# Optimization experiments

Hardware: AMD Instinct MI355X
Metric: run time of the kernel (lower is better)

The kernel has to match this reference:

```python
import jax, jax.numpy as jnp
import numpy as np

N, E, B = 20000, 60000, 512
F_IN, ED, H, C = 7, 3, 4, 256
HC = H * C  # 1024
D_MODEL = 1024
EPS_BN = 1e-5


def setup_inputs() -> dict:
    key = jax.random.key(0)
    ks = jax.random.split(key, 24)
    s = 0.05
    inp = {
        'x': jax.random.normal(ks[0], (N, F_IN), jnp.float32),
        'edge_index': jax.random.randint(ks[1], (2, E), 0, N, jnp.int32),
        'edge_attr': jax.random.normal(ks[2], (E, ED), jnp.float32),
        'batch': jnp.sort(jax.random.randint(ks[3], (N,), 0, B, jnp.int32)),
        'w0': jax.random.normal(ks[4], (F_IN, HC), jnp.float32) * s,
        'w_rest': jax.random.normal(ks[5], (3, HC, HC), jnp.float32) * s,
        'w_edge': jax.random.normal(ks[6], (4, ED, HC), jnp.float32) * s,
        'att_src': jax.random.normal(ks[7], (4, H, C), jnp.float32) * s,
        'att_dst': jax.random.normal(ks[8], (4, H, C), jnp.float32) * s,
        'att_edge': jax.random.normal(ks[9], (4, H, C), jnp.float32) * s,
        'bias012': jax.random.normal(ks[10], (3, HC), jnp.float32) * s,
        'bias3': jax.random.normal(ks[11], (C,), jnp.float32) * s,
        'bn_gamma': jnp.ones((3, HC), jnp.float32),
        'bn_beta': jnp.zeros((3, HC), jnp.float32),
        'bn_mean': jnp.zeros((3, HC), jnp.float32),
        'bn_var': jnp.ones((3, HC), jnp.float32),
        'gate_w': jax.random.normal(ks[12], (C, 1), jnp.float32) * s,
        'gate_b': jnp.zeros((1,), jnp.float32),
        'proj_w': jax.random.normal(ks[13], (C, D_MODEL), jnp.float32) * s,
        'proj_b': jnp.zeros((D_MODEL,), jnp.float32),
    }
    return inp


def _gat_layer(x, ei, ea, W, We, a_s, a_d, a_e, bias, concat):
    # PyG GATConv with edge_dim, add_self_loops=True (fill_value='mean'), eval mode (no dropout)
    n = x.shape[0]
    sl = jnp.arange(n, dtype=ei.dtype)
    ea_mean = ea.mean(axis=0)
    ei = jnp.concatenate([ei, jnp.stack([sl, sl])], axis=1)            # [2, E+N]
    ea = jnp.concatenate([ea, jnp.broadcast_to(ea_mean, (n, ea.shape[1]))], axis=0)
    h = (x @ W).reshape(n, H, C)                                       # [N,H,C]
    alpha_src = jnp.einsum('nhc,hc->nh', h, a_s)
    alpha_dst = jnp.einsum('nhc,hc->nh', h, a_d)
    eh = (ea @ We).reshape(-1, H, C)
    alpha_e = jnp.einsum('ehc,hc->eh', eh, a_e)
    src, dst = ei[0], ei[1]
    alpha = jax.nn.leaky_relu(alpha_src[src] + alpha_dst[dst] + alpha_e, 0.2)  # [E+N,H]
    amax = jax.ops.segment_max(alpha, dst, num_segments=n)
    alpha = jnp.exp(alpha - amax[dst])
    denom = jax.ops.segment_sum(alpha, dst, num_segments=n)
    alpha = alpha / (denom[dst] + 1e-16)
    msg = h[src] * alpha[:, :, None]                                   # [E+N,H,C]
    out = jax.ops.segment_sum(msg, dst, num_segments=n)                # [N,H,C]
    out = out.reshape(n, H * C) if concat else out.mean(axis=1)
    return out + bias


def reference(x, edge_index, edge_attr, batch, w0, w_rest, w_edge, att_src, att_dst,
              att_edge, bias012, bias3, bn_gamma, bn_beta, bn_mean, bn_var,
              gate_w, gate_b, proj_w, proj_b):
    h = x
    for i in range(4):
        W = w0 if i == 0 else w_rest[i - 1]
        concat = i < 3
        b = bias012[i] if concat else bias3
        h = _gat_layer(h, edge_index, edge_attr, W, w_edge[i],
                       att_src[i], att_dst[i], att_edge[i], b, concat)
        if i < 3:
            # BatchNorm1d in eval mode, then ReLU (dropout is identity in eval)
            h = (h - bn_mean[i]) * (bn_gamma[i] / jnp.sqrt(bn_var[i] + EPS_BN)) + bn_beta[i]
            h = jax.nn.relu(h)
    # AttentionalAggregation: segment softmax over gate scores, weighted sum per graph
    gate = h @ gate_w + gate_b                                         # [N,1]
    gmax = jax.ops.segment_max(gate, batch, num_segments=B)
    g = jnp.exp(gate - gmax[batch])
    gsum = jax.ops.segment_sum(g, batch, num_segments=B)
    w = g / (gsum[batch] + 1e-16)
    graph = jax.ops.segment_sum(w * h, batch, num_segments=B)          # [B,256]
    return graph @ proj_w + proj_b                                     # [B,1024]
```

## Files before the change

### kernel.cpp

```cpp
#include <hip/hip_runtime.h>
#include <math.h>

#define NN 20000
#define NP 20480
#define EE 60000
#define BB 512
#define HC 1024
#define HH 4
#define CC 256

typedef _Float16 f16;
typedef f16 half8 __attribute__((ext_vector_type(8)));
typedef f16 f16x4 __attribute__((ext_vector_type(4)));
typedef float floatx4 __attribute__((ext_vector_type(4)));
typedef float floatx16 __attribute__((ext_vector_type(16)));

__device__ __forceinline__ size_t af_off(int n, int c) {
    int mblk = n >> 7, rr = n & 127;
    int iter = c >> 5, kc = c & 31;
    int kh = kc >> 4, kg = (kc >> 3) & 1, e = kc & 7;
    return ((((size_t)(mblk * 32 + iter) * 2 + kh) * 4 + (rr >> 5)) * 64 +
            (kg * 32 + (rr & 31))) * 8 + e;
}

__device__ __forceinline__ int node_remap(int bid) {
    return (bid >> 3) + (bid & 7) * 2500;
}

__device__ __forceinline__ void gload16(const f16* g, f16* l) {
    __builtin_amdgcn_global_load_lds((const __attribute__((address_space(1))) void*)g,
                                     (__attribute__((address_space(3))) void*)l, 16, 0, 0);
}

__global__ void ehist_kernel(const float* __restrict__ ea, const int* __restrict__ ei,
                             float* sums, int* counts, int E_) {
    int e = blockIdx.x * 256 + threadIdx.x;
    float s0 = 0.f, s1 = 0.f, s2 = 0.f;
    if (e < E_) {
        atomicAdd(&counts[ei[E_ + e]], 1);
        s0 = ea[e * 3 + 0];
        s1 = ea[e * 3 + 1];
        s2 = ea[e * 3 + 2];
    }
    for (int o = 32; o; o >>= 1) {
        s0 += __shfl_down(s0, o);
        s1 += __shfl_down(s1, o);
        s2 += __shfl_down(s2, o);
    }
    if ((threadIdx.x & 63) == 0) {
        atomicAdd(&sums[0], s0);
        atomicAdd(&sums[1], s1);
        atomicAdd(&sums[2], s2);
    }
}

__global__ void scan1_kernel(const int* __restrict__ counts, int* __restrict__ partial,
                             int* __restrict__ psums, int n) {
    __shared__ int sdata[256];
    int t = threadIdx.x;
    int i = blockIdx.x * 256 + t;
    int v = (i < n) ? counts[i] : 0;
    sdata[t] = v;
    __syncthreads();
#pragma unroll
    for (int off = 1; off < 256; off <<= 1) {
        int tmp = (t >= off) ? sdata[t - off] : 0;
        __syncthreads();
        sdata[t] += tmp;
        __syncthreads();
    }
    if (i < n) partial[i] = sdata[t];
    if (t == 255) psums[blockIdx.x] = sdata[255];
}

__global__ void scan2_kernel(int* __restrict__ psums, int nb) {
    __shared__ int sdata[128];
    int t = threadIdx.x;
    sdata[t] = (t < nb) ? psums[t] : 0;
    __syncthreads();
#pragma unroll
    for (int off = 1; off < 128; off <<= 1) {
        int tmp = (t >= off) ? sdata[t - off] : 0;
        __syncthreads();
        sdata[t] += tmp;
        __syncthreads();
    }
    if (t < nb) psums[t] = (t == 0) ? 0 : sdata[t - 1];
}

__global__ void scan3_kernel(const int* __restrict__ partial, const int* __restrict__ psums,
                             int* __restrict__ indptr, int n) {
    int i = blockIdx.x * 256 + threadIdx.x;
    if (i == 0) indptr[0] = 0;
    if (i < n) indptr[i + 1] = partial[i] + psums[blockIdx.x];
}

__global__ void scatter_kernel(const int* __restrict__ ei, const int* __restrict__ indptr,
                               int* fill, int* sorted, int* sdst, int E_) {
    int e = blockIdx.x * 256 + threadIdx.x;
    if (e >= E_) return;
    int d = ei[E_ + e];
    int pos = indptr[d] + atomicAdd(&fill[d], 1);
    sorted[pos] = e;
    sdst[pos] = d;
}

__global__ void bptr_kernel(const int* __restrict__ batch, int* bptr, int n, int nb) {
    int i = blockIdx.x * 256 + threadIdx.x;
    if (i >= n) return;
    int b = batch[i];
    if (i == 0) {
        for (int bb = 0; bb <= b; bb++) bptr[bb] = 0;
    } else {
        int pb = batch[i - 1];
        if (pb != b) {
            for (int bb = pb + 1; bb <= b; bb++) bptr[bb] = i;
        }
    }
    if (i == n - 1) {
        for (int bb = b + 1; bb <= nb; bb++) bptr[bb] = n;
    }
}

__global__ void prep0_kernel(const float* __restrict__ w_rest, f16* __restrict__ Bf,
                             const float* __restrict__ att_src,
                             const float* __restrict__ att_dst,
                             const float* __restrict__ w0,
                             const float* __restrict__ bias012, const float* __restrict__ bn_g,
                             const float* __restrict__ bn_b, const float* __restrict__ bn_m,
                             const float* __restrict__ bn_v,
                             const float* __restrict__ w_edge,
                             const float* __restrict__ att_edge,
                             const float* __restrict__ ea_sums,
                             float* __restrict__ wsv, float* __restrict__ wdv,
                             float* __restrict__ w0s, float* __restrict__ w0d,
                             float2* __restrict__ bnss,
                             float* __restrict__ Mmat, float* __restrict__ ae_self,
                             float invE) {
    int bid = blockIdx.x;
    int t = threadIdx.x;
    if (bid < 768) {
        __shared__ float tile[64][65];
        int bx = (bid & 15) * 64;
        int by = ((bid >> 4) & 15) * 64;
        int l = bid >> 8;
        int tr = t >> 6, tc = t & 63;
#pragma unroll
        for (int i = 0; i < 16; i++) {
            int r = by + i * 4 + tr;
            tile[i * 4 + tr][tc] = w_rest[(size_t)l * 1048576 + (size_t)r * 1024 + bx + tc];
        }
        __syncthreads();
        f16* bl = Bf + (size_t)l * 1048576;
#pragma unroll
        for (int ii = 0; ii < 2; ii++) {
            int idx = ii * 256 + t;
            int nl = idx >> 3, kg8 = idx & 7;
            int n = bx + nl, k = by + kg8 * 8;
            half8 v;
#pragma unroll
            for (int e = 0; e < 8; e++) v[e] = (f16)tile[kg8 * 8 + e][nl];
            *(half8*)&bl[af_off(n, k)] = v;
        }
    } else if (bid < 3840) {
        int b = bid - 768;
        int l = b >> 10, k = b & 1023;
        int hp = t >> 6, lane = t & 63;
        int col = hp * 256 + lane * 4;
        const float* wrow = w_rest + (size_t)l * 1048576 + (size_t)k * 1024;
        float4 w4 = *(const float4*)&wrow[col];
        float4 a4 = *(const float4*)&att_src[(l + 1) * HC + col];
        float4 d4 = *(const float4*)&att_dst[(l + 1) * HC + col];
        float sp = w4.x * a4.x + w4.y * a4.y + w4.z * a4.z + w4.w * a4.w;
        float dp = w4.x * d4.x + w4.y * d4.y + w4.z * d4.z + w4.w * d4.w;
        for (int m = 1; m < 64; m <<= 1) {
            sp += __shfl_xor(sp, m);
            dp += __shfl_xor(dp, m);
        }
        if (lane == 0) {
            wsv[((size_t)l * 1024 + k) * 4 + hp] = sp;
            wdv[((size_t)l * 1024 + k) * 4 + hp] = dp;
        }
    } else if (bid < 3847) {
        int f = bid - 3840;
        int hp = t >> 6, lane = t & 63;
        int col = hp * 256 + lane * 4;
        float4 w4 = *(const float4*)&w0[f * HC + col];
        float4 a4 = *(const float4*)&att_src[col];
        float4 d4 = *(const float4*)&att_dst[col];
        float sp = w4.x * a4.x + w4.y * a4.y + w4.z * a4.z + w4.w * a4.w;
        float dp = w4.x * d4.x + w4.y * d4.y + w4.z * d4.z + w4.w * d4.w;
        for (int m = 1; m < 64; m <<= 1) {
            sp += __shfl_xor(sp, m);
            dp += __shfl_xor(dp, m);
        }
        if (lane == 0) {
            w0s[f * 4 + hp] = sp;
            w0d[f * 4 + hp] = dp;
        }
    } else if (bid < 3859) {
        int i = (bid - 3847) * 256 + t;
        if (i < 3 * HC) {
            float s = bn_g[i] * rsqrtf(bn_v[i] + 1e-5f);
            float2 o;
            o.x = s;
            o.y = (bias012[i] - bn_m[i]) * s + bn_b[i];
            bnss[i] = o;
        }
    } else {
        __shared__ float red[256];
        __shared__ float Ms[12];
        int l = bid - 3859;
        for (int dh = 0; dh < 12; dh++) {
            int d = dh >> 2, hh = dh & 3;
            float v = w_edge[l * 3072 + d * HC + hh * CC + t] *
                      att_edge[l * HC + hh * CC + t];
            red[t] = v;
            __syncthreads();
            for (int o = 128; o; o >>= 1) {
                if (t < o) red[t] += red[t + o];
                __syncthreads();
            }
            if (t == 0) {
                Ms[dh] = red[0];
                Mmat[l * 12 + dh] = red[0];
            }
            __syncthreads();
        }
        if (t < 4) {
            float v = 0.f;
            for (int d = 0; d < 3; d++) v += ea_sums[d] * invE * Ms[d * 4 + t];
            ae_self[l * 4 + t] = v;
        }
    }
}

__global__ void prep2_kernel(const int* __restrict__ ei, const int* __restrict__ sorted,
                             const float* __restrict__ ea, const float* __restrict__ Mmat,
                             int* __restrict__ ssrc, float* __restrict__ aeh_pk,
                             const float* __restrict__ x, const float* __restrict__ w0s,
                             const float* __restrict__ w0d, float* __restrict__ asrc,
                             float* __restrict__ adst, float* __restrict__ xpad) {
    int bid = blockIdx.x;
    int t = threadIdx.x;
    if (bid < 235) {
        int idx = bid * 256 + t;
        if (idx >= EE) return;
        int eid = sorted[idx];
        ssrc[idx] = ei[eid];
        float a0 = ea[eid * 3 + 0], a1 = ea[eid * 3 + 1], a2 = ea[eid * 3 + 2];
#pragma unroll
        for (int l = 0; l < 4; l++) {
#pragma unroll
            for (int h = 0; h < 4; h++) {
                aeh_pk[(size_t)idx * 16 + l * 4 + h] =
                    a0 * Mmat[l * 12 + h] + a1 * Mmat[l * 12 + 4 + h] +
                    a2 * Mmat[l * 12 + 8 + h];
            }
        }
    } else {
        int n = (bid - 235) * 256 + t;
        if (n >= NN) return;
        float xr[7];
#pragma unroll
        for (int f = 0; f < 7; f++) xr[f] = x[n * 7 + f];
        float4 p0, p1;
        p0.x = xr[0]; p0.y = xr[1]; p0.z = xr[2]; p0.w = xr[3];
        p1.x = xr[4]; p1.y = xr[5]; p1.z = xr[6]; p1.w = 0.f;
        *(float4*)&xpad[(size_t)n * 8] = p0;
        *(float4*)&xpad[(size_t)n * 8 + 4] = p1;
#pragma unroll
        for (int hp = 0; hp < 4; hp++) {
            float s = 0.f, d = 0.f;
#pragma unroll
            for (int f = 0; f < 7; f++) {
                s += xr[f] * w0s[f * 4 + hp];
                d += xr[f] * w0d[f * 4 + hp];
            }
            asrc[n * 4 + hp] = s;
            adst[n * 4 + hp] = d;
        }
    }
}

__global__ void edgep_kernel(const int* __restrict__ ssrc, const int* __restrict__ sdst,
                             const float* __restrict__ aeh_pk, const float* __restrict__ asrc,
                             const float* __restrict__ adst, float* __restrict__ pe,
                             int layer) {
    int i = blockIdx.x * 256 + threadIdx.x;
    if (i >= EE) return;
    int src = ssrc[i];
    int dst = sdst[i];
    float4 a = *(const float4*)&asrc[(size_t)src * 4];
    float4 d = *(const float4*)&adst[(size_t)dst * 4];
    float4 m = *(const float4*)&aeh_pk[(size_t)i * 16 + layer * 4];
    float r[4] = {a.x + d.x + m.x, a.y + d.y + m.y, a.z + d.z + m.z, a.w + d.w + m.w};
    float4 o;
#pragma unroll
    for (int k = 0; k < 4; k++) {
        float v = (r[k] > 0.f) ? r[k] : 0.2f * r[k];
        (&o.x)[k] = __expf(v);
    }
    *(float4*)&pe[(size_t)i * 4] = o;
}

__global__ void agg0x_kernel(const float* __restrict__ xpad, const float* __restrict__ asrc,
                             const float* __restrict__ adst, const float* __restrict__ ae_self,
                             const int* __restrict__ ssrc, const float* __restrict__ pe,
                             const int* __restrict__ indptr, float* __restrict__ xagg) {
    int n = blockIdx.x * 256 + threadIdx.x;
    if (n >= NN) return;
    float4 as4 = *(const float4*)&asrc[(size_t)n * 4];
    float4 ad4 = *(const float4*)&adst[(size_t)n * 4];
    float adl[4] = {ad4.x, ad4.y, ad4.z, ad4.w};
    float asl[4] = {as4.x, as4.y, as4.z, as4.w};
    float4 x0 = *(const float4*)&xpad[(size_t)n * 8];
    float4 x1 = *(const float4*)&xpad[(size_t)n * 8 + 4];
    float xr[7] = {x0.x, x0.y, x0.z, x0.w, x1.x, x1.y, x1.z};
    float denom[4];
    float xa[4][7];
#pragma unroll
    for (int h = 0; h < 4; h++) {
        float r = asl[h] + adl[h] + ae_self[h];
        r = (r > 0.f) ? r : 0.2f * r;
        float p = __expf(r);
        denom[h] = p;
#pragma unroll
        for (int f = 0; f < 7; f++) xa[h][f] = p * xr[f];
    }
    int s = indptr[n], e = indptr[n + 1];
    for (int idx = s; idx < e; idx++) {
        int src = ssrc[idx];
        float4 pv = *(const float4*)&pe[(size_t)idx * 4];
        float pl[4] = {pv.x, pv.y, pv.z, pv.w};
        float4 s0 = *(const float4*)&xpad[(size_t)src * 8];
        float4 s1 = *(const float4*)&xpad[(size_t)src * 8 + 4];
        float xs[7] = {s0.x, s0.y, s0.z, s0.w, s1.x, s1.y, s1.z};
#pragma unroll
        for (int h = 0; h < 4; h++) {
            denom[h] += pl[h];
#pragma unroll
            for (int f = 0; f < 7; f++) xa[h][f] += pl[h] * xs[f];
        }
    }
#pragma unroll
    for (int h = 0; h < 4; h++) {
        float inv = 1.0f / (denom[h] + 1e-16f);
#pragma unroll
        for (int f = 0; f < 7; f++) xagg[(size_t)n * 28 + h * 7 + f] = xa[h][f] * inv;
    }
}

__global__ void gemm7f_kernel(const float* __restrict__ xagg, const float* __restrict__ w0,
                              const float2* __restrict__ bnss, const float* __restrict__ wsv,
                              const float* __restrict__ wdv, f16* __restrict__ outAf,
                              float* __restrict__ asrc_n, float* __restrict__ adst_n) {
    __shared__ float xs[28];
    __shared__ float red[32];
    int n = node_remap(blockIdx.x);
    int t = threadIdx.x;
    if (t < 28) xs[t] = xagg[(size_t)n * 28 + t];
    __syncthreads();
    int head = t >> 6;
    int j0 = t * 4;
    float sp[4] = {0.f, 0.f, 0.f, 0.f}, dp[4] = {0.f, 0.f, 0.f, 0.f};
    f16x4 o;
#pragma unroll
    for (int k = 0; k < 4; k++) {
        int j = j0 + k;
        float dot = 0.f;
#pragma unroll
        for (int f = 0; f < 7; f++) dot += xs[head * 7 + f] * w0[f * HC + j];
        float2 ss = bnss[j];
        float val = fmaxf(fmaf(dot, ss.x, ss.y), 0.f);
        o[k] = (f16)val;
        float4 w4s = *(const float4*)&wsv[(size_t)j * 4];
        float4 w4d = *(const float4*)&wdv[(size_t)j * 4];
        sp[0] += val * w4s.x; sp[1] += val * w4s.y;
        sp[2] += val * w4s.z; sp[3] += val * w4s.w;
        dp[0] += val * w4d.x; dp[1] += val * w4d.y;
        dp[2] += val * w4d.z; dp[3] += val * w4d.w;
    }
    *(f16x4*)&outAf[af_off(n, j0)] = o;
    int wave = t >> 6, lane = t & 63;
#pragma unroll
    for (int m = 1; m < 64; m <<= 1) {
#pragma unroll
        for (int j = 0; j < 4; j++) {
            sp[j] += __shfl_xor(sp[j], m);
            dp[j] += __shfl_xor(dp[j], m);
        }
    }
    if (lane == 0) {
#pragma unroll
        for (int j = 0; j < 4; j++) {
            red[wave * 8 + j] = sp[j];
            red[wave * 8 + 4 + j] = dp[j];
        }
    }
    __syncthreads();
    if (t < 8) {
        float v = red[t] + red[8 + t] + red[16 + t] + red[24 + t];
        if (t < 4) asrc_n[n * 4 + t] = v;
        else adst_n[n * 4 + (t - 4)] = v;
    }
}

#define EPB 235
__global__ __launch_bounds__(256) void gemmep_kernel(
    const f16* __restrict__ Af, const f16* __restrict__ Bf, f16* __restrict__ C16,
    const int* __restrict__ ssrc, const int* __restrict__ sdst,
    const float* __restrict__ aeh_pk, const float* __restrict__ asrc,
    const float* __restrict__ adst, float* __restrict__ pe, int layer) {
    __shared__ __align__(16) f16 lds[16384];
    int t = threadIdx.x;
    int bid = blockIdx.x;
    if (bid < EPB) {
        int i = bid * 256 + t;
        if (i >= EE) return;
        int src = ssrc[i];
        int dst = sdst[i];
        float4 a = *(const float4*)&asrc[(size_t)src * 4];
        float4 d = *(const float4*)&adst[(size_t)dst * 4];
        float4 m = *(const float4*)&aeh_pk[(size_t)i * 16 + layer * 4];
        float r[4] = {a.x + d.x + m.x, a.y + d.y + m.y, a.z + d.z + m.z, a.w + d.w + m.w};
        float4 o;
#pragma unroll
        for (int k = 0; k < 4; k++) {
            float v = (r[k] > 0.f) ? r[k] : 0.2f * r[k];
            (&o.x)[k] = __expf(v);
        }
        *(float4*)&pe[(size_t)i * 4] = o;
        return;
    }
    int gid = bid - EPB;
    int w = t >> 6, lane = t & 63;
    int g = gid >> 6, rblk = gid & 63;
    int nblk = rblk >> 3;
    int mblk = g * 8 + (rblk & 7);
    int rg0 = (w >> 1) * 2;
    int cg0 = (w & 1) * 2;

    floatx16 acc[2][2];
#pragma unroll
    for (int i = 0; i < 2; i++)
#pragma unroll
        for (int j = 0; j < 2; j++) acc[i][j] = (floatx16)(0.f);

    const f16* ga0 = Af + (size_t)mblk * 131072 + w * 1024 + lane * 8;
    const f16* gb0 = Bf + (size_t)nblk * 131072 + w * 1024 + lane * 8;

    auto STAGE = [&](int it, int b) {
        const f16* ga = ga0 + (size_t)it * 4096;
        const f16* gb = gb0 + (size_t)it * 4096;
        f16* la = &lds[b * 8192 + w * 1024 + lane * 8];
        f16* lb = &lds[b * 8192 + 4096 + w * 1024 + lane * 8];
        gload16(ga, la);
        gload16(ga + 512, la + 512);
        gload16(gb, lb);
        gload16(gb + 512, lb + 512);
    };
    auto COMPUTE = [&](int b) {
        half8 afr[2][2], bfr[2][2];
#pragma unroll
        for (int kh = 0; kh < 2; kh++) {
#pragma unroll
            for (int i = 0; i < 2; i++) {
                afr[kh][i] = *(const half8*)&lds[b * 8192 + kh * 2048 + (rg0 + i) * 512 +
                                                 lane * 8];
                bfr[kh][i] = *(const half8*)&lds[b * 8192 + 4096 + kh * 2048 +
                                                 (cg0 + i) * 512 + lane * 8];
            }
        }
#pragma unroll
        for (int kh = 0; kh < 2; kh++)
#pragma unroll
            for (int i = 0; i < 2; i++)
#pragma unroll
                for (int j = 0; j < 2; j++)
                    acc[i][j] = __builtin_amdgcn_mfma_f32_32x32x16_f16(bfr[kh][j], afr[kh][i],
                                                                       acc[i][j], 0, 0, 0);
    };

    STAGE(0, 0);
    __syncthreads();
#pragma unroll 1
    for (int k2 = 0; k2 < 16; k2++) {
        int i0 = k2 * 2;
        STAGE(i0 + 1, 1);
        COMPUTE(0);
        __syncthreads();
        if (i0 + 2 < 32) STAGE(i0 + 2, 0);
        COMPUTE(1);
        __syncthreads();
    }

    int fr32 = lane & 31, kg = lane >> 5;
#pragma unroll
    for (int i = 0; i < 2; i++) {
        int row = mblk * 128 + rg0 * 32 + i * 32 + fr32;
#pragma unroll
        for (int j = 0; j < 2; j++) {
#pragma unroll
            for (int gq = 0; gq < 4; gq++) {
                f16x4 o;
#pragma unroll
                for (int r = 0; r < 4; r++) o[r] = (f16)acc[i][j][gq * 4 + r];
                *(f16x4*)&C16[(size_t)row * HC + nblk * 128 + cg0 * 32 + j * 32 + gq * 8 +
                              kg * 4] = o;
            }
        }
    }
}

__global__ void agg_kernel(const f16* __restrict__ h16, const float* __restrict__ asrc,
                           const float* __restrict__ adst, const float* __restrict__ ae_self,
                           const int* __restrict__ ssrc, const float* __restrict__ pe,
                           const int* __restrict__ indptr, const float2* __restrict__ bnss,
                           const float* __restrict__ wsv, const float* __restrict__ wdv,
                           const float* __restrict__ bias3, const float* __restrict__ gw,
                           const float* __restrict__ gb, f16* __restrict__ out16,
                           float* __restrict__ asrc_n, float* __restrict__ adst_n,
                           float* __restrict__ out3, float* __restrict__ gate,
                           int layer, int concat) {
    __shared__ float buf[1024];
    __shared__ float red[32];
    int n = node_remap(blockIdx.x);
    int t = threadIdx.x;
    int h = t >> 6, lane = t & 63;
    int c4 = t * 4;

    float r = asrc[n * 4 + h] + adst[n * 4 + h] + ae_self[layer * 4 + h];
    r = (r > 0.f) ? r : 0.2f * r;
    float p = __expf(r);
    float denom = p;
    float ax, ay, az, aw;
    {
        f16x4 v = *(const f16x4*)&h16[(size_t)n * HC + c4];
        ax = p * (float)v[0]; ay = p * (float)v[1];
        az = p * (float)v[2]; aw = p * (float)v[3];
    }
    int s = indptr[n], epos = indptr[n + 1];
    for (int base = s; base < epos; base += 4) {
        int rem = epos - base;
        int src[4];
        float pv[4];
#pragma unroll
        for (int j = 0; j < 4; j++) {
            if (j < rem) {
                src[j] = ssrc[base + j];
                pv[j] = pe[(size_t)(base + j) * 4 + h];
            } else {
                src[j] = n;
                pv[j] = 0.f;
            }
        }
        f16x4 u[4];
#pragma unroll
        for (int j = 0; j < 4; j++) u[j] = *(const f16x4*)&h16[(size_t)src[j] * HC + c4];
#pragma unroll
        for (int j = 0; j < 4; j++) {
            denom += pv[j];
            ax += pv[j] * (float)u[j][0];
            ay += pv[j] * (float)u[j][1];
            az += pv[j] * (float)u[j][2];
            aw += pv[j] * (float)u[j][3];
        }
    }
    float inv = 1.0f / (denom + 1e-16f);
    ax *= inv; ay *= inv; az *= inv; aw *= inv;

    if (concat) {
        float vals[4] = {ax, ay, az, aw};
        f16x4 o;
        float sp[4] = {0.f, 0.f, 0.f, 0.f}, dp[4] = {0.f, 0.f, 0.f, 0.f};
#pragma unroll
        for (int k = 0; k < 4; k++) {
            int j = c4 + k;
            float2 ss = bnss[j];
            float val = fmaxf(fmaf(vals[k], ss.x, ss.y), 0.f);
            o[k] = (f16)val;
            float4 w4s = *(const float4*)&wsv[(size_t)j * 4];
            float4 w4d = *(const float4*)&wdv[(size_t)j * 4];
            sp[0] += val * w4s.x; sp[1] += val * w4s.y;
            sp[2] += val * w4s.z; sp[3] += val * w4s.w;
            dp[0] += val * w4d.x; dp[1] += val * w4d.y;
            dp[2] += val * w4d.z; dp[3] += val * w4d.w;
        }
        *(f16x4*)&out16[af_off(n, c4)] = o;
#pragma unroll
        for (int m = 1; m < 64; m <<= 1) {
#pragma unroll
            for (int j = 0; j < 4; j++) {
                sp[j] += __shfl_xor(sp[j], m);
                dp[j] += __shfl_xor(dp[j], m);
            }
        }
        if (lane == 0) {
#pragma unroll
            for (int j = 0; j < 4; j++) {
                red[h * 8 + j] = sp[j];
                red[h * 8 + 4 + j] = dp[j];
            }
        }
        __syncthreads();
        if (t < 8) {
            float v = red[t] + red[8 + t] + red[16 + t] + red[24 + t];
            if (t < 4) asrc_n[n * 4 + t] = v;
            else adst_n[n * 4 + (t - 4)] = v;
        }
    } else {
        buf[c4 + 0] = ax;
        buf[c4 + 1] = ay;
        buf[c4 + 2] = az;
        buf[c4 + 3] = aw;
        __syncthreads();
        if (t < 64) {
            float gpart = 0.f;
#pragma unroll
            for (int k = 0; k < 4; k++) {
                int c = t * 4 + k;
                float v2 = 0.25f * (buf[c] + buf[256 + c] + buf[512 + c] + buf[768 + c]) +
                           bias3[c];
                out3[(size_t)n * CC + c] = v2;
                gpart += v2 * gw[c];
            }
            for (int o = 32; o; o >>= 1) gpart += __shfl_down(gpart, o);
            if (t == 0) gate[n] = gpart + gb[0];
        }
    }
}

__global__ void graphagg_kernel(const float* __restrict__ gate, const float* __restrict__ h3,
                                const int* __restrict__ bptr, float* __restrict__ graph) {
    __shared__ float red[256];
    __shared__ float wn[256];
    int b = blockIdx.x, t = threadIdx.x;
    int s = bptr[b], epos = bptr[b + 1];
    float m = -3.4e38f;
    for (int n = s + t; n < epos; n += 256) m = fmaxf(m, gate[n]);
    red[t] = m;
    __syncthreads();
    for (int o = 128; o; o >>= 1) {
        if (t < o) red[t] = fmaxf(red[t], red[t + o]);
        __syncthreads();
    }
    float mval = red[0];
    __syncthreads();
    float sum = 0.f;
    for (int n = s + t; n < epos; n += 256) sum += __expf(gate[n] - mval);
    red[t] = sum;
    __syncthreads();
    for (int o = 128; o; o >>= 1) {
        if (t < o) red[t] += red[t + o];
        __syncthreads();
    }
    float ssum = red[0];
    __syncthreads();
    float acc = 0.f;
    for (int base = s; base < epos; base += 256) {
        int n = base + t;
        wn[t] = (n < epos) ? __expf(gate[n] - mval) : 0.f;
        __syncthreads();
        int cnt = min(256, epos - base);
        for (int j = 0; j < cnt; j++) acc += wn[j] * h3[(size_t)(base + j) * CC + t];
        __syncthreads();
    }
    graph[b * CC + t] = acc / (ssum + 1e-16f);
}

__global__ void proj_kernel(const float* __restrict__ graph, const float* __restrict__ pw,
                            const float* __restrict__ pb, float* __restrict__ out) {
    __shared__ float g[8][256];
    int b = blockIdx.x, t = threadIdx.x;
#pragma unroll
    for (int r = 0; r < 8; r++) g[r][t] = graph[(size_t)(b * 8 + r) * 256 + t];
    __syncthreads();
    float acc[8][4];
#pragma unroll
    for (int r = 0; r < 8; r++)
#pragma unroll
        for (int q = 0; q < 4; q++) acc[r][q] = pb[t + q * 256];
    for (int c = 0; c < 256; c++) {
        float w[4];
#pragma unroll
        for (int q = 0; q < 4; q++) w[q] = pw[(size_t)c * 1024 + t + q * 256];
#pragma unroll
        for (int r = 0; r < 8; r++) {
            float gv = g[r][c];
#pragma unroll
            for (int q = 0; q < 4; q++) acc[r][q] += gv * w[q];
        }
    }
#pragma unroll
    for (int r = 0; r < 8; r++)
#pragma unroll
        for (int q = 0; q < 4; q++)
            out[(size_t)(b * 8 + r) * 1024 + t + q * 256] = acc[r][q];
}

extern "C" void kernel_launch(void* const* d_in, const int* in_sizes, int n_in,
                              void* d_out, int out_size, void* d_ws, size_t ws_size,
                              hipStream_t stream) {
    const float* x = (const float*)d_in[0];
    const int* ei = (const int*)d_in[1];
    const float* ea = (const float*)d_in[2];
    const int* batch = (const int*)d_in[3];
    const float* w0 = (const float*)d_in[4];
    const float* w_rest = (const float*)d_in[5];
    const float* w_edge = (const float*)d_in[6];
    const float* att_src = (const float*)d_in[7];
    const float* att_dst = (const float*)d_in[8];
    const float* att_edge = (const float*)d_in[9];
    const float* bias012 = (const float*)d_in[10];
    const float* bias3 = (const float*)d_in[11];
    const float* bn_g = (const float*)d_in[12];
    const float* bn_b = (const float*)d_in[13];
    const float* bn_m = (const float*)d_in[14];
    const float* bn_v = (const float*)d_in[15];
    const float* gate_w = (const float*)d_in[16];
    const float* gate_b = (const float*)d_in[17];
    const float* proj_w = (const float*)d_in[18];
    const float* proj_b = (const float*)d_in[19];
    float* out = (float*)d_out;

    float* ws = (float*)d_ws;
    size_t off = 0;
    f16* h_lin = (f16*)(ws + off); off += (size_t)NP * HC / 2;
    f16* h_af = (f16*)(ws + off); off += (size_t)NP * HC / 2;
    float* h3 = ws + off; off += (size_t)NN * CC;
    f16* Bf = (f16*)(ws + off); off += (size_t)3 * HC * HC / 2;
    float* xpad = ws + off; off += (size_t)NN * 8;
    float* asrcA = ws + off; off += (size_t)NN * 4;
    float* adstA = ws + off; off += (size_t)NN * 4;
    float* asrcB = ws + off; off += (size_t)NN * 4;
    float* adstB = ws + off; off += (size_t)NN * 4;
    float* wsv = ws + off; off += (size_t)3 * HC * 4;
    float* wdv = ws + off; off += (size_t)3 * HC * 4;
    float* w0s = ws + off; off += 28;
    float* w0d = ws + off; off += 28;
    float2* bnss = (float2*)(ws + off); off += (size_t)3 * HC * 2;
    float* aeh_pk = ws + off; off += (size_t)EE * 16;
    float* pbuf = ws + off; off += (size_t)EE * 4;
    float* xagg = ws + off; off += (size_t)NN * 28;
    float* gate = ws + off; off += (size_t)NN;
    float* graph = ws + off; off += (size_t)BB * CC;
    float* ea_sums = ws + off; off += 4;
    float* Mmat = ws + off; off += 48;
    float* ae_self = ws + off; off += 16;
    int* counts = (int*)(ws + off); off += NN;
    int* partial = (int*)(ws + off); off += NN;
    int* psums = (int*)(ws + off); off += 128;
    int* indptr = (int*)(ws + off); off += NN + 1;
    int* fill = (int*)(ws + off); off += NN;
    int* sorted = (int*)(ws + off); off += EE;
    int* ssrc = (int*)(ws + off); off += EE;
    int* sdst = (int*)(ws + off); off += EE;
    int* bptr = (int*)(ws + off); off += BB + 1;

    hipMemsetAsync(ea_sums, 0, 4 * sizeof(float), stream);
    hipMemsetAsync(counts, 0, NN * sizeof(int), stream);
    hipMemsetAsync(fill, 0, NN * sizeof(int), stream);

    ehist_kernel<<<(EE + 255) / 256, 256, 0, stream>>>(ea, ei, ea_sums, counts, EE);
    int nblk = (NN + 255) / 256;
    scan1_kernel<<<nblk, 256, 0, stream>>>(counts, partial, psums, NN);
    scan2_kernel<<<1, 128, 0, stream>>>(psums, nblk);
    scan3_kernel<<<nblk, 256, 0, stream>>>(partial, psums, indptr, NN);
    scatter_kernel<<<(EE + 255) / 256, 256, 0, stream>>>(ei, indptr, fill, sorted, sdst, EE);
    bptr_kernel<<<(NN + 255) / 256, 256, 0, stream>>>(batch, bptr, NN, BB);
    prep0_kernel<<<3863, 256, 0, stream>>>(w_rest, Bf, att_src, att_dst, w0, bias012, bn_g,
                                           bn_b, bn_m, bn_v, w_edge, att_edge, ea_sums,
                                           wsv, wdv, w0s, w0d, bnss, Mmat, ae_self,
                                           1.0f / EE);
    prep2_kernel<<<235 + nblk, 256, 0, stream>>>(ei, sorted, ea, Mmat, ssrc, aeh_pk,
                                                 x, w0s, w0d, asrcA, adstA, xpad);

    edgep_kernel<<<(EE + 255) / 256, 256, 0, stream>>>(ssrc, sdst, aeh_pk, asrcA, adstA,
                                                       pbuf, 0);
    agg0x_kernel<<<nblk, 256, 0, stream>>>(xpad, asrcA, adstA, ae_self, ssrc,
                                           pbuf, indptr, xagg);
    gemm7f_kernel<<<NN, 256, 0, stream>>>(xagg, w0, bnss, wsv, wdv, h_af, asrcB, adstB);

    float* asrc_cur = asrcB;
    float* adst_cur = adstB;
    float* asrc_nxt = asrcA;
    float* adst_nxt = adstA;
    for (int i = 1; i < 4; i++) {
        gemmep_kernel<<<EPB + (NP / 128) * (HC / 128), 256, 0, stream>>>(
            h_af, Bf + (size_t)(i - 1) * HC * HC, h_lin,
            ssrc, sdst, aeh_pk, asrc_cur, adst_cur, pbuf, i);
        agg_kernel<<<NN, 256, 0, stream>>>(
            h_lin, asrc_cur, adst_cur, ae_self, ssrc, pbuf, indptr, bnss + (size_t)i * HC,
            wsv + (size_t)i * HC * 4, wdv + (size_t)i * HC * 4, bias3, gate_w, gate_b,
            h_af, asrc_nxt, adst_nxt, h3, gate, i, (i < 3) ? 1 : 0);
        float* tmp = asrc_cur; asrc_cur = asrc_nxt; asrc_nxt = tmp;
        tmp = adst_cur; adst_cur = adst_nxt; adst_nxt = tmp;
    }

    graphagg_kernel<<<BB, 256, 0, stream>>>(gate, h3, bptr, graph);
    proj_kernel<<<BB / 8, 256, 0, stream>>>(graph, proj_w, proj_b, out);
}
```

Baseline: 651.8 us.

## Process 32 nodes per block in layer-0 transform kernel with fragment-layout stores

Rewrites gemm7f so each 256-thread block handles 32 nodes instead of one. Each wave covers one head and writes 8-wide f16 vectors straight in the MFMA A-fragment layout, and the attention dot products are reduced with a single shuffle plus a shared-memory cross-wave sum. The aim is to cut per-node block launch and sync overhead, reuse the w0/bnss/wsv reads across many nodes, and make stores coalesced. It drops node_remap and assumes N is a multiple of 32 and that the 128-row fragment blocks line up with the 32-node groups.

```diff
diff --git a/kernel.cpp b/kernel.cpp
--- a/kernel.cpp
+++ b/kernel.cpp
@@ -355,54 +355,72 @@
                               const float2* __restrict__ bnss, const float* __restrict__ wsv,
                               const float* __restrict__ wdv, f16* __restrict__ outAf,
                               float* __restrict__ asrc_n, float* __restrict__ adst_n) {
-    __shared__ float xs[28];
-    __shared__ float red[32];
-    int n = node_remap(blockIdx.x);
+    __shared__ float xs[32][29];
+    __shared__ float red[4][32][8];
+    int bid = blockIdx.x;
     int t = threadIdx.x;
-    if (t < 28) xs[t] = xagg[(size_t)n * 28 + t];
-    __syncthreads();
-    int head = t >> 6;
-    int j0 = t * 4;
+    int n0 = bid * 32;
+    int mblk = bid >> 2, rg = bid & 3;
+    for (int i = t; i < 896; i += 256) xs[i / 28][i % 28] = xagg[(size_t)n0 * 28 + i];
+    __syncthreads();
+    int w = t >> 6, lane = t & 63;
+    int lr = lane & 31, kg = lane >> 5;
+    float x7[7];
+#pragma unroll
+    for (int f = 0; f < 7; f++) x7[f] = xs[lr][w * 7 + f];
     float sp[4] = {0.f, 0.f, 0.f, 0.f}, dp[4] = {0.f, 0.f, 0.f, 0.f};
-    f16x4 o;
-#pragma unroll
-    for (int k = 0; k < 4; k++) {
-        int j = j0 + k;
-        float dot = 0.f;
-#pragma unroll
-        for (int f = 0; f < 7; f++) dot += xs[head * 7 + f] * w0[f * HC + j];
-        float2 ss = bnss[j];
-        float val = fmaxf(fmaf(dot, ss.x, ss.y), 0.f);
-        o[k] = (f16)val;
-        float4 w4s = *(const float4*)&wsv[(size_t)j * 4];
-        float4 w4d = *(const float4*)&wdv[(size_t)j * 4];
-        sp[0] += val * w4s.x; sp[1] += val * w4s.y;
-        sp[2] += val * w4s.z; sp[3] += val * w4s.w;
-        dp[0] += val * w4d.x; dp[1] += val * w4d.y;
-        dp[2] += val * w4d.z; dp[3] += val * w4d.w;
-    }
-    *(f16x4*)&outAf[af_off(n, j0)] = o;
-    int wave = t >> 6, lane = t & 63;
-#pragma unroll
-    for (int m = 1; m < 64; m <<= 1) {
-#pragma unroll
-        for (int j = 0; j < 4; j++) {
-            sp[j] += __shfl_xor(sp[j], m);
-            dp[j] += __shfl_xor(dp[j], m);
-        }
-    }
-    if (lane == 0) {
-#pragma unroll
-        for (int j = 0; j < 4; j++) {
-            red[wave * 8 + j] = sp[j];
-            red[wave * 8 + 4 + j] = dp[j];
-        }
-    }
-    __syncthreads();
-    if (t < 8) {
-        float v = red[t] + red[8 + t] + red[16 + t] + red[24 + t];
-        if (t < 4) asrc_n[n * 4 + t] = v;
-        else adst_n[n * 4 + (t - 4)] = v;
+#pragma unroll
+    for (int p = 0; p < 16; p++) {
+        int iter = w * 8 + (p >> 1);
+        int kh = p & 1;
+        int c0 = iter * 32 + (kh * 2 + kg) * 8;
+        float dot[8];
+#pragma unroll
+        for (int e = 0; e < 8; e++) dot[e] = 0.f;
+#pragma unroll
+        for (int f = 0; f < 7; f++) {
+            float4 wa = *(const float4*)&w0[f * HC + c0];
+            float4 wb = *(const float4*)&w0[f * HC + c0 + 4];
+            dot[0] += x7[f] * wa.x; dot[1] += x7[f] * wa.y;
+            dot[2] += x7[f] * wa.z; dot[3] += x7[f] * wa.w;
+            dot[4] += x7[f] * wb.x; dot[5] += x7[f] * wb.y;
+            dot[6] += x7[f] * wb.z; dot[7] += x7[f] * wb.w;
+        }
+        half8 o;
+#pragma unroll
+        for (int e = 0; e < 8; e++) {
+            int j = c0 + e;
+            float2 ss = bnss[j];
+            float val = fmaxf(fmaf(dot[e], ss.x, ss.y), 0.f);
+            o[e] = (f16)val;
+            float4 w4s = *(const float4*)&wsv[(size_t)j * 4];
+            float4 w4d = *(const float4*)&wdv[(size_t)j * 4];
+            sp[0] += val * w4s.x; sp[1] += val * w4s.y;
+            sp[2] += val * w4s.z; sp[3] += val * w4s.w;
+            dp[0] += val * w4d.x; dp[1] += val * w4d.y;
+            dp[2] += val * w4d.z; dp[3] += val * w4d.w;
+        }
+        size_t off = ((((size_t)(mblk * 32 + iter) * 2 + kh) * 4 + rg) * 64 + lane) * 8;
+        *(half8*)&outAf[off] = o;
+    }
+#pragma unroll
+    for (int q = 0; q < 4; q++) {
+        sp[q] += __shfl_xor(sp[q], 32);
+        dp[q] += __shfl_xor(dp[q], 32);
+    }
+    if (kg == 0) {
+#pragma unroll
+        for (int q = 0; q < 4; q++) {
+            red[w][lr][q] = sp[q];
+            red[w][lr][4 + q] = dp[q];
+        }
+    }
+    __syncthreads();
+    {
+        int lr2 = t >> 3, q = t & 7;
+        float v = red[0][lr2][q] + red[1][lr2][q] + red[2][lr2][q] + red[3][lr2][q];
+        if (q < 4) asrc_n[(size_t)(n0 + lr2) * 4 + q] = v;
+        else adst_n[(size_t)(n0 + lr2) * 4 + (q - 4)] = v;
     }
 }
 
@@ -780,7 +798,8 @@
                                                        pbuf, 0);
     agg0x_kernel<<<nblk, 256, 0, stream>>>(xpad, asrcA, adstA, ae_self, ssrc,
                                            pbuf, indptr, xagg);
-    gemm7f_kernel<<<NN, 256, 0, stream>>>(xagg, w0, bnss, wsv, wdv, h_af, asrcB, adstB);
+    gemm7f_kernel<<<NN / 32, 256, 0, stream>>>(xagg, w0, bnss, wsv, wdv, h_af, asrcB,
+                                               adstB);
 
     float* asrc_cur = asrcB;
     float* adst_cur = adstB;
```

After: 623.7 us. -4.3%, faster.
